# Optimization experiments

Measured on AMD Instinct MI355X. Metric: run time of the kernel, lower is better.

The kernel has to match this reference:

```python
import jax, jax.numpy as jnp
import numpy as np

D_MODEL = 1024
NHEAD = 16
D_K = D_MODEL // NHEAD
CHUNK = 256


def setup_inputs() -> dict:
    key = jax.random.key(0)
    ks = jax.random.split(key, 11)
    S, B = 4096, 4
    inp = {
        "query": jax.random.normal(ks[0], (S, B, D_MODEL), dtype=jnp.float32),
        "key": jax.random.normal(ks[1], (S, B, D_MODEL), dtype=jnp.float32),
        "value": jax.random.normal(ks[2], (S, B, D_MODEL), dtype=jnp.float32),
        # nn.Linear params: y = x @ W.T + b
        "Wq": jax.random.normal(ks[3], (D_MODEL, D_MODEL), dtype=jnp.float32) * 0.02,
        "bq": jnp.zeros((D_MODEL,), dtype=jnp.float32),
        "Wk": jax.random.normal(ks[4], (D_MODEL, D_MODEL), dtype=jnp.float32) * 0.02,
        "bk": jnp.zeros((D_MODEL,), dtype=jnp.float32),
        "Wv": jax.random.normal(ks[5], (D_MODEL, D_MODEL), dtype=jnp.float32) * 0.02,
        "bv": jnp.zeros((D_MODEL,), dtype=jnp.float32),
        "Wo": jax.random.normal(ks[6], (D_MODEL, D_MODEL), dtype=jnp.float32) * 0.02,
        "bo": jnp.zeros((D_MODEL,), dtype=jnp.float32),
    }
    return inp


def _split_heads(x, B):
    # (S, B, D) -> (B, H, S, d_k)
    S = x.shape[0]
    return x.reshape(S, B, NHEAD, D_K).transpose(1, 2, 0, 3)


def reference(query, key, value, Wq, bq, Wk, bk, Wv, bv, Wo, bo):
    S, B, _ = query.shape
    n_chunks = S // CHUNK  # S assumed divisible by CHUNK

    q = _split_heads(query @ Wq.T + bq, B)  # (B,H,S,dk)
    k = _split_heads(key @ Wk.T + bk, B)
    v = _split_heads(value @ Wv.T + bv, B)

    # Block-diagonal attention: softmax is strictly within each chunk.
    qc = q.reshape(B, NHEAD, n_chunks, CHUNK, D_K)
    kc = k.reshape(B, NHEAD, n_chunks, CHUNK, D_K)
    vc = v.reshape(B, NHEAD, n_chunks, CHUNK, D_K)

    scale = 1.0 / np.sqrt(D_K).astype(np.float32)
    scores = jnp.einsum("bhncd,bhnkd->bhnck", qc, kc) * scale  # (B,H,n,C,C)
    probs = jax.nn.softmax(scores, axis=-1)
    out = jnp.einsum("bhnck,bhnkd->bhncd", probs, vc)  # (B,H,n,C,dk)

    # (B,H,S,dk) -> (S,B,H*dk)
    out = out.reshape(B, NHEAD, S, D_K).transpose(2, 0, 1, 3).reshape(S, B, D_MODEL)
    return out @ Wo.T + bo
```

## Files before the change

kernel.cpp:

```cpp
#include <hip/hip_runtime.h>
#include <hip/hip_bf16.h>


namespace {

constexpr int kSeq = 4096, kB = 4, kDm = 1024, kNh = 16, kDk = 64, kChk = 256;
constexpr int kMr = kSeq * kB;
constexpr float kLog2e = 1.44269504088896340736f;

typedef __attribute__((ext_vector_type(8))) short bf16x8;
typedef __attribute__((ext_vector_type(4))) short bf16x4;
typedef __attribute__((ext_vector_type(4))) float f32x4;
typedef __attribute__((ext_vector_type(8))) unsigned short u16x8;
typedef __attribute__((ext_vector_type(4))) unsigned short u16x4;

#define AS1 __attribute__((address_space(1)))
#define AS3 __attribute__((address_space(3)))

__device__ __forceinline__ unsigned short f2bf(float x) {
  union { float f; unsigned u; } v; v.f = x;
  unsigned r = v.u + 0x7fffu + ((v.u >> 16) & 1u);
  return (unsigned short)(r >> 16);
}
__device__ __forceinline__ unsigned cvtpk(float lo, float hi) {
  unsigned r;
  asm("v_cvt_pk_bf16_f32 %0, %1, %2" : "=v"(r) : "v"(lo), "v"(hi));
  return r;
}
__device__ __forceinline__ int swz(int bo) { return bo ^ ((bo >> 3) & 0x70); }

__device__ __forceinline__ f32x4 mfma16x16(bf16x4 a, bf16x4 b, f32x4 c) {
#if __has_builtin(__builtin_amdgcn_mfma_f32_16x16x16bf16_1k)
  return __builtin_amdgcn_mfma_f32_16x16x16bf16_1k(a, b, c, 0, 0, 0);
#else
  asm volatile("v_mfma_f32_16x16x16_bf16 %0, %1, %2, %0\n\ts_nop 4"
               : "+v"(c) : "v"(a), "v"(b));
  return c;
#endif
}

__global__ __launch_bounds__(256) void cvt4(const float* __restrict__ s0,
                                            const float* __restrict__ s1,
                                            const float* __restrict__ s2,
                                            const float* __restrict__ s3,
                                            unsigned short* __restrict__ dst) {
  int i = blockIdx.x * 256 + threadIdx.x;
  int t = i >> 18;
  int j = i & 0x3ffff;
  const float* s = (t == 0) ? s0 : (t == 1) ? s1 : (t == 2) ? s2 : s3;
  f32x4 v = *(const f32x4*)(s + (size_t)j * 4);
  u16x4 o;
  o[0] = f2bf(v[0]); o[1] = f2bf(v[1]); o[2] = f2bf(v[2]); o[3] = f2bf(v[3]);
  *(u16x4*)(dst + (size_t)i * 4) = o;
}

__global__ __launch_bounds__(256) void cvt3(const float* __restrict__ s0,
                                            const float* __restrict__ s1,
                                            const float* __restrict__ s2,
                                            unsigned short* __restrict__ dst) {
  size_t i = (size_t)blockIdx.x * 256 + threadIdx.x;
  int t = (int)(i >> 22);
  size_t j = i & 0x3fffff;
  const float* s = (t == 0) ? s0 : (t == 1) ? s1 : s2;
  f32x4 v = *(const f32x4*)(s + j * 4);
  u16x4 o;
  o[0] = f2bf(v[0]); o[1] = f2bf(v[1]); o[2] = f2bf(v[2]); o[3] = f2bf(v[3]);
  *(u16x4*)(dst + i * 4) = o;
}

__global__ __launch_bounds__(512, 2) void gemm_qkv8(
    const unsigned short* __restrict__ qbf, const unsigned short* __restrict__ kbf,
    const unsigned short* __restrict__ vbf, const unsigned short* __restrict__ Wcat,
    const float* __restrict__ bq, const float* __restrict__ bk,
    const float* __restrict__ bv, unsigned short* __restrict__ dst, float sQ) {
  constexpr int K = kDm, nkt = K / 64;
  __shared__ unsigned short sh[65536];
  const int tid = (int)threadIdx.x;
  const int l = tid & 63;
  const int l15 = l & 15, l4 = l >> 4, l7 = l15 & 7;
  const int wid = tid >> 6, wm = wid >> 2, wn = wid & 3, wn1 = wn & 1;
  const int bid = (int)blockIdx.x;
  const int xcd = bid & 7, idx = bid >> 3;
  const int rbi = xcd * 8 + (idx & 7);
  const int cbi = idx >> 3;
  const int mat = cbi >> 2, ccol = (cbi & 3) * 256;
  const float* bp = (mat == 0) ? bq : (mat == 1) ? bk : bv;
  const float scale = (mat == 0) ? sQ : 1.0f;
  const unsigned short* Ain = (mat == 0) ? qbf : (mat == 1) ? kbf : vbf;
  unsigned short* out = dst + (size_t)mat * kMr * kDm;

  const int srow = tid >> 3;
  const int g16 = (tid & 7) ^ (srow & 7);
  const unsigned short* gA = Ain + (size_t)(rbi * 256 + srow) * K + g16 * 8;
  const unsigned short* gB = Wcat + (size_t)(cbi * 256 + srow) * K + g16 * 8;
  const int ldsbase = (tid & ~63) * 8;

  auto stageA = [&](int T, int h) {
    const unsigned short* s = gA + (size_t)h * (128 * K) + T * 64;
    unsigned short* d = sh + ((T & 1) * 2 + h) * 8192 + ldsbase;
    __builtin_amdgcn_global_load_lds((const AS1 unsigned int*)s, (AS3 unsigned int*)d, 16, 0, 0);
    __builtin_amdgcn_global_load_lds((const AS1 unsigned int*)(s + 64 * K),
                                     (AS3 unsigned int*)(d + 4096), 16, 0, 0);
  };
  auto stageB = [&](int T, int h) {
    const unsigned short* s = gB + (size_t)h * (128 * K) + T * 64;
    unsigned short* d = sh + 32768 + ((T & 1) * 2 + h) * 8192 + ldsbase;
    __builtin_amdgcn_global_load_lds((const AS1 unsigned int*)s, (AS3 unsigned int*)d, 16, 0, 0);
    __builtin_amdgcn_global_load_lds((const AS1 unsigned int*)(s + 64 * K),
                                     (AS3 unsigned int*)(d + 4096), 16, 0, 0);
  };

  f32x4 acc[8][4] = {};
  bf16x8 bfr[4];

  stageB(0, 0); stageB(0, 1);
  stageA(0, 0); stageA(0, 1);
  stageB(1, 0); stageB(1, 1);
  asm volatile("s_waitcnt vmcnt(4)" ::: "memory");
  __builtin_amdgcn_s_barrier();

  for (int it = 0; it < nkt / 2; ++it) {
#pragma unroll
    for (int tt = 0; tt < 2; ++tt) {
      const int T = 2 * it + tt;
      const unsigned short* Asl = sh + ((T & 1) * 2 + wm) * 8192;
      const unsigned short* Bsl = sh + 32768 + ((T & 1) * 2 + (wn >> 1)) * 8192;
#pragma unroll
      for (int p = 0; p < 4; ++p) {
        const int kk = p >> 1, mfh = p & 1;
        bf16x8 af[4];
        const int sc = ((kk * 4 + l4) ^ l7) * 8;
        if (mfh == 0) {
#pragma unroll
          for (int nf = 0; nf < 4; ++nf)
            bfr[nf] = *(const bf16x8*)&Bsl[(wn1 * 64 + nf * 16 + l15) * 64 + sc];
        }
#pragma unroll
        for (int i = 0; i < 4; ++i)
          af[i] = *(const bf16x8*)&Asl[(mfh * 64 + i * 16 + l15) * 64 + sc];
        if (p == 0 && T + 1 < nkt) stageA(T + 1, 0);
        if (p == 1 && T + 1 < nkt) stageA(T + 1, 1);
        if (p == 3 && T + 2 < nkt) { stageB(T + 2, 0); stageB(T + 2, 1); }
        __builtin_amdgcn_s_barrier();
        __builtin_amdgcn_s_setprio(1);
#pragma unroll
        for (int i = 0; i < 4; ++i)
#pragma unroll
          for (int nf = 0; nf < 4; ++nf)
            acc[mfh * 4 + i][nf] =
                __builtin_amdgcn_mfma_f32_16x16x32_bf16(af[i], bfr[nf], acc[mfh * 4 + i][nf], 0, 0, 0);
        __builtin_amdgcn_s_setprio(0);
        if (p == 3 && T + 1 < nkt) {
          if (T + 2 < nkt) asm volatile("s_waitcnt vmcnt(4)" ::: "memory");
          else             asm volatile("s_waitcnt vmcnt(0)" ::: "memory");
        }
        __builtin_amdgcn_s_barrier();
      }
    }
  }

#pragma unroll
  for (int mf = 0; mf < 8; ++mf)
#pragma unroll
    for (int nf = 0; nf < 4; ++nf) {
      int col = wn * 64 + nf * 16 + l15;
      float bvv = bp[ccol + col];
      int grpc = col >> 6;
      int c16 = (col & 63) >> 3, pos = col & 7;
#pragma unroll
      for (int j = 0; j < 4; ++j) {
        int tl = wm * 128 + mf * 16 + l4 * 4 + j;
        int grp = (tl & 3) * 4 + grpc;
        int u = (tl >> 2) * 8 + c16;
        int byte = (grp * 8192 + u * 16 + pos * 2) ^ (((u >> 3) & 7) << 4);
        *(unsigned short*)((char*)sh + byte) = f2bf((acc[mf][nf][j] + bvv) * scale);
      }
    }
  __syncthreads();
  {
    int inner = tid & 31, grp = tid >> 5;
    int b2 = grp >> 2, hl = grp & 3;
    int h = (cbi & 3) * 4 + hl;
    unsigned short* po = out + ((size_t)(b2 * kNh + h) * kSeq + rbi * 64) * kDk;
#pragma unroll
    for (int i = 0; i < 16; ++i) {
      int u = i * 32 + inner;
      int byte = (grp * 8192 + u * 16) ^ (((u >> 3) & 7) << 4);
      u16x8 v = *(const u16x8*)((const char*)sh + byte);
      *(u16x8*)(po + u * 8) = v;
    }
  }
}

__global__ __launch_bounds__(256) void gemm_o(const unsigned short* __restrict__ Aw,
                                              const unsigned short* __restrict__ Bw,
                                              const float* __restrict__ bias,
                                              float* __restrict__ Cp) {
  constexpr int K = kDm, N = kDm;
  __shared__ unsigned short sh[20480];
  const int tid = (int)threadIdx.x;
  const int l = tid & 63;
  const int wbase = tid & ~63;
  const int bid = (int)blockIdx.x;
  const int lin = (bid & 7) * 128 + (bid >> 3);
  const int rb = (lin >> 3) * 128, cb = (lin & 7) * 128;
  const int wr = ((tid >> 7) & 1) * 64;
  const int wc = ((tid >> 6) & 1) * 64;
  const int l15 = l & 15, l4 = l >> 4;

  const int rr0 = tid >> 2;
  const int c4p = (tid & 3) ^ (rr0 & 3);
  const int t0 = rb + rr0, t1 = t0 + 64;
  const unsigned short* gA0 =
      Aw + ((size_t)((t0 & 3) * kNh) * kSeq + (t0 >> 2)) * kDk + c4p * 8;
  const unsigned short* gA1 =
      Aw + ((size_t)((t1 & 3) * kNh) * kSeq + (t1 >> 2)) * kDk + c4p * 8;
  const unsigned short* gB0 = Bw + (size_t)(cb + rr0) * K + c4p * 8;
  const unsigned short* gB1 = gB0 + (size_t)64 * K;
  const int rchk = (l4 ^ (l15 & 3)) * 8;

  f32x4 acc[4][4] = {};

  auto stageA = [&](int slot, int kt) {
    unsigned short* d = sh + slot * 4096;
    size_t ko = (size_t)(kt >> 1) * ((size_t)kSeq * kDk) + (kt & 1) * 32;
    __builtin_amdgcn_global_load_lds((const AS1 unsigned int*)(gA0 + ko),
                                     (AS3 unsigned int*)&d[wbase * 8], 16, 0, 0);
    __builtin_amdgcn_global_load_lds((const AS1 unsigned int*)(gA1 + ko),
                                     (AS3 unsigned int*)&d[(256 + wbase) * 8], 16, 0, 0);
  };
  auto stageB = [&](int slot, int kt) {
    unsigned short* d = sh + 8192 + slot * 4096;
    __builtin_amdgcn_global_load_lds((const AS1 unsigned int*)(gB0 + kt * 32),
                                     (AS3 unsigned int*)&d[wbase * 8], 16, 0, 0);
    __builtin_amdgcn_global_load_lds((const AS1 unsigned int*)(gB1 + kt * 32),
                                     (AS3 unsigned int*)&d[(256 + wbase) * 8], 16, 0, 0);
  };

  constexpr int nkt = K >> 5;
  stageA(0, 0); stageB(0, 0); stageB(1, 1);
  asm volatile("s_waitcnt vmcnt(2)" ::: "memory");
  __builtin_amdgcn_s_barrier();
  __builtin_amdgcn_sched_barrier(0);

  int aR = 0, bR = 0;
  for (int kt = 0; kt < nkt; ++kt) {
    if (kt + 1 < nkt) stageA(aR ^ 1, kt + 1);
    if (kt + 2 < nkt) { int bW = bR + 2; if (bW >= 3) bW -= 3; stageB(bW, kt + 2); }
    const unsigned short* AsC = sh + aR * 4096;
    const unsigned short* BsC = sh + 8192 + bR * 4096;
    bf16x8 af[4], bfr[4];
#pragma unroll
    for (int m = 0; m < 4; ++m)
      af[m] = *(const bf16x8*)&AsC[(wr + m * 16 + l15) * 32 + rchk];
#pragma unroll
    for (int n = 0; n < 4; ++n)
      bfr[n] = *(const bf16x8*)&BsC[(wc + n * 16 + l15) * 32 + rchk];
#pragma unroll
    for (int m = 0; m < 4; ++m)
#pragma unroll
      for (int n = 0; n < 4; ++n)
        acc[m][n] = __builtin_amdgcn_mfma_f32_16x16x32_bf16(af[m], bfr[n], acc[m][n], 0, 0, 0);
    if (kt + 1 < nkt) {
      if (kt + 2 < nkt) asm volatile("s_waitcnt vmcnt(2)" ::: "memory");
      else              asm volatile("s_waitcnt vmcnt(0)" ::: "memory");
      __builtin_amdgcn_s_barrier();
      __builtin_amdgcn_sched_barrier(0);
    }
    aR ^= 1;
    bR = (bR + 1 == 3) ? 0 : bR + 1;
  }

#pragma unroll
  for (int n = 0; n < 4; ++n) {
    int col = cb + wc + n * 16 + l15;
    float bvv = bias[col];
#pragma unroll
    for (int m = 0; m < 4; ++m) {
      int row0 = rb + wr + m * 16 + l4 * 4;
#pragma unroll
      for (int j = 0; j < 4; ++j)
        Cp[(size_t)(row0 + j) * N + col] = acc[m][n][j] + bvv;
    }
  }
}

template <int ALAY, int OHM>
__global__ __launch_bounds__(256) void gemm_bt(const void* __restrict__ Ap,
                                               const unsigned short* __restrict__ Bw,
                                               const float* __restrict__ bias,
                                               void* __restrict__ Cp, float scale) {
  constexpr int K = kDm, N = kDm;
  __shared__ unsigned short As[2][128 * 32];
  __shared__ unsigned short Bs[2][128 * 32];
  const int tid = (int)threadIdx.x;
  const int l = tid & 63;
  const int wbase = tid & ~63;
  const int bid = (int)blockIdx.x;
  const int lin = (bid & 7) * 128 + (bid >> 3);
  const int rb = (lin >> 3) * 128, cb = (lin & 7) * 128;
  const int wr = ((tid >> 7) & 1) * 64;
  const int wc = ((tid >> 6) & 1) * 64;
  const int l15 = l & 15, l4 = l >> 4;

  f32x4 acc[4][4] = {};

  auto stage = [&](int buf, int k0) {
    if constexpr (ALAY == 1) {
      const float* A = (const float*)Ap;
#pragma unroll
      for (int i = 0; i < 4; ++i) {
        int ci = tid + 256 * i;
        int rr = ci >> 3, c4 = ci & 7;
        f32x4 v = *(const f32x4*)(A + (size_t)(rb + rr) * K + (k0 + c4 * 4));
        u16x4 o;
        o[0] = f2bf(v[0]); o[1] = f2bf(v[1]); o[2] = f2bf(v[2]); o[3] = f2bf(v[3]);
        *(u16x4*)&As[buf][rr * 32 + c4 * 4] = o;
      }
    } else {
      const unsigned short* A = (const unsigned short*)Ap;
      int h = k0 >> 6, d0 = k0 & 63;
#pragma unroll
      for (int i = 0; i < 2; ++i) {
        int ch = i * 256 + tid;
        int rr = ch >> 2, cc = ch & 3;
        int t = rb + rr; int s = t >> 2, b2 = t & 3;
        const unsigned short* g =
            A + ((size_t)(b2 * kNh + h) * kSeq + s) * kDk + d0 + cc * 8;
        __builtin_amdgcn_global_load_lds((const AS1 unsigned int*)g,
                                         (AS3 unsigned int*)&As[buf][(i * 256 + wbase) * 8],
                                         16, 0, 0);
      }
    }
#pragma unroll
    for (int i = 0; i < 2; ++i) {
      int ch = i * 256 + tid;
      int rr = ch >> 2, cc = ch & 3;
      const unsigned short* g = Bw + (size_t)(cb + rr) * K + (k0 + cc * 8);
      __builtin_amdgcn_global_load_lds((const AS1 unsigned int*)g,
                                       (AS3 unsigned int*)&Bs[buf][(i * 256 + wbase) * 8],
                                       16, 0, 0);
    }
  };

  stage(0, 0);
  __syncthreads();
  int cur = 0;
  constexpr int nkt = K >> 5;
  for (int kt = 0; kt < nkt; ++kt) {
    if (kt + 1 < nkt) stage(cur ^ 1, (kt + 1) << 5);
    bf16x8 af[4], bfr[4];
#pragma unroll
    for (int m = 0; m < 4; ++m)
      af[m] = *(const bf16x8*)&As[cur][(wr + m * 16 + l15) * 32 + l4 * 8];
#pragma unroll
    for (int n = 0; n < 4; ++n)
      bfr[n] = *(const bf16x8*)&Bs[cur][(wc + n * 16 + l15) * 32 + l4 * 8];
#pragma unroll
    for (int m = 0; m < 4; ++m)
#pragma unroll
      for (int n = 0; n < 4; ++n)
        acc[m][n] = __builtin_amdgcn_mfma_f32_16x16x32_bf16(af[m], bfr[n], acc[m][n], 0, 0, 0);
    __syncthreads();
    cur ^= 1;
  }

#pragma unroll
  for (int n = 0; n < 4; ++n) {
    int col = cb + wc + n * 16 + l15;
    float bvv = bias[col];
    int h = col >> 6, dd = col & 63;
#pragma unroll
    for (int m = 0; m < 4; ++m) {
      int row0 = rb + wr + m * 16 + l4 * 4;
#pragma unroll
      for (int j = 0; j < 4; ++j) {
        float v = acc[m][n][j] + bvv;
        int t = row0 + j;
        if constexpr (OHM) {
          int s = t >> 2, b2 = t & 3;
          ((unsigned short*)Cp)[((size_t)(b2 * kNh + h) * kSeq + s) * kDk + dd] =
              f2bf(v * scale);
        } else {
          ((float*)Cp)[(size_t)t * N + col] = v;
        }
      }
    }
  }
}

__global__ __launch_bounds__(256) void attn_blkdiag(const unsigned short* __restrict__ qw,
                                                    const unsigned short* __restrict__ kw,
                                                    const unsigned short* __restrict__ vw,
                                                    unsigned short* __restrict__ ow) {
  __shared__ unsigned short Kl[64 * 64];
  __shared__ unsigned short Vt[64 * 64];
  const int tid = (int)threadIdx.x;
  const int w = tid >> 6, l = tid & 63;
  const int l15 = l & 15, l4 = l >> 4;
  const int bid0 = (int)blockIdx.x;
  const int bid = (bid0 & 7) * 256 + (bid0 >> 3);
  const int hf = bid & 1, c = (bid >> 1) & 15, bh = bid >> 5;
  const size_t base = ((size_t)bh * kSeq + c * kChk) * kDk;
  const unsigned short* qp = qw + base + (size_t)hf * 128 * kDk;
  const unsigned short* kp = kw + base;
  const unsigned short* vp = vw + base;

  bf16x8 q[2][2];
#pragma unroll
  for (int m = 0; m < 2; ++m)
#pragma unroll
    for (int kk = 0; kk < 2; ++kk)
      q[m][kk] = *(const bf16x8*)(qp + (w * 32 + m * 16 + l15) * 64 + kk * 32 + l4 * 8);

  float mst[2] = {-1e30f, -1e30f}, lst[2] = {0.f, 0.f};
  f32x4 oacc[2][4] = {};

  const int r = tid >> 2, c0 = (tid & 3) * 16;
  u16x8 kr0, kr1, vr0, vr1;
  {
    const unsigned short* kt = kp + tid * 16;
    kr0 = *(const u16x8*)kt; kr1 = *(const u16x8*)(kt + 8);
    const unsigned short* vt = vp + tid * 16;
    vr0 = *(const u16x8*)vt; vr1 = *(const u16x8*)(vt + 8);
  }

  for (int kb = 0; kb < 4; ++kb) {
    __syncthreads();
    {
      int bo = r * 128 + c0 * 2;
      *(u16x8*)((char*)Kl + swz(bo)) = kr0;
      *(u16x8*)((char*)Kl + swz(bo + 16)) = kr1;
#pragma unroll
      for (int j = 0; j < 8; ++j) {
        *(unsigned short*)((char*)Vt + swz((c0 + j) * 128 + r * 2)) = vr0[j];
        *(unsigned short*)((char*)Vt + swz((c0 + 8 + j) * 128 + r * 2)) = vr1[j];
      }
    }
    __syncthreads();
    if (kb < 3) {
      const unsigned short* kt = kp + (kb + 1) * (64 * kDk) + tid * 16;
      kr0 = *(const u16x8*)kt; kr1 = *(const u16x8*)(kt + 8);
      const unsigned short* vt = vp + (kb + 1) * (64 * kDk) + tid * 16;
      vr0 = *(const u16x8*)vt; vr1 = *(const u16x8*)(vt + 8);
    }

    f32x4 sacc[4][2] = {};
    __builtin_amdgcn_s_setprio(1);
#pragma unroll
    for (int kk = 0; kk < 2; ++kk) {
      bf16x8 kf[4];
#pragma unroll
      for (int kn = 0; kn < 4; ++kn) {
        int bo = (kn * 16 + l15) * 128 + (kk * 32 + l4 * 8) * 2;
        kf[kn] = *(const bf16x8*)((const char*)Kl + swz(bo));
      }
#pragma unroll
      for (int kn = 0; kn < 4; ++kn)
#pragma unroll
        for (int m = 0; m < 2; ++m)
          sacc[kn][m] = __builtin_amdgcn_mfma_f32_16x16x32_bf16(kf[kn], q[m][kk], sacc[kn][m], 0, 0, 0);
    }
    __builtin_amdgcn_s_setprio(0);

    unsigned pw[2][4][2];
    float cbq[2][4];
#pragma unroll
    for (int m = 0; m < 2; ++m) {
      float rm = -1e30f;
#pragma unroll
      for (int kn = 0; kn < 4; ++kn)
#pragma unroll
        for (int j = 0; j < 4; ++j) rm = fmaxf(rm, sacc[kn][m][j]);
      rm = fmaxf(rm, __shfl_xor(rm, 16, 64));
      rm = fmaxf(rm, __shfl_xor(rm, 32, 64));
      float mn = fmaxf(mst[m], rm);
      float corr = exp2f(mst[m] - mn);
      mst[m] = mn;
      float rs = 0.f;
#pragma unroll
      for (int kn = 0; kn < 4; ++kn) {
#pragma unroll
        for (int j = 0; j < 4; ++j) {
          float p = exp2f(sacc[kn][m][j] - mn);
          sacc[kn][m][j] = p;
          rs += p;
        }
        pw[m][kn][0] = cvtpk(sacc[kn][m][0], sacc[kn][m][1]);
        pw[m][kn][1] = cvtpk(sacc[kn][m][2], sacc[kn][m][3]);
      }
      rs += __shfl_xor(rs, 16, 64);
      rs += __shfl_xor(rs, 32, 64);
      lst[m] = lst[m] * corr + rs;
#pragma unroll
      for (int j = 0; j < 4; ++j) cbq[m][j] = __shfl(corr, l4 * 4 + j, 64);
#pragma unroll
      for (int n = 0; n < 4; ++n)
#pragma unroll
        for (int j = 0; j < 4; ++j) oacc[m][n][j] *= cbq[m][j];
    }

    __builtin_amdgcn_s_setprio(1);
#pragma unroll
    for (int kn = 0; kn < 4; ++kn) {
      bf16x4 vf[4];
#pragma unroll
      for (int n = 0; n < 4; ++n) {
        int bo = (n * 16 + l15) * 128 + (kn * 16 + l4 * 4) * 2;
        vf[n] = *(const bf16x4*)((const char*)Vt + swz(bo));
      }
#pragma unroll
      for (int m = 0; m < 2; ++m) {
        union { unsigned u[2]; bf16x4 h; } pk;
        pk.u[0] = pw[m][kn][0]; pk.u[1] = pw[m][kn][1];
#pragma unroll
        for (int n = 0; n < 4; ++n)
          oacc[m][n] = mfma16x16(pk.h, vf[n], oacc[m][n]);
      }
    }
    __builtin_amdgcn_s_setprio(0);
  }

  unsigned short* op = ow + base + (size_t)hf * 128 * kDk;
#pragma unroll
  for (int m = 0; m < 2; ++m) {
    float inv = 1.f / lst[m];
#pragma unroll
    for (int j = 0; j < 4; ++j) {
      float ib = __shfl(inv, l4 * 4 + j, 64);
      int srow = w * 32 + m * 16 + l4 * 4 + j;
#pragma unroll
      for (int n = 0; n < 4; ++n)
        op[(size_t)srow * 64 + n * 16 + l15] = f2bf(oacc[m][n][j] * ib);
    }
  }
}

}

extern "C" void kernel_launch(void* const* d_in, const int* in_sizes, int n_in,
                              void* d_out, int out_size, void* d_ws, size_t ws_size,
                              hipStream_t stream) {
  const float* query = (const float*)d_in[0];
  const float* key   = (const float*)d_in[1];
  const float* value = (const float*)d_in[2];
  const float* Wq = (const float*)d_in[3];
  const float* bq = (const float*)d_in[4];
  const float* Wk = (const float*)d_in[5];
  const float* bk = (const float*)d_in[6];
  const float* Wv = (const float*)d_in[7];
  const float* bv = (const float*)d_in[8];
  const float* Wo = (const float*)d_in[9];
  const float* bo = (const float*)d_in[10];

  const float sQ = 0.125f * kLog2e;

  const size_t wsz = (size_t)kDm * kDm;
  const size_t tsz = (size_t)kMr * kDm;
  unsigned short* wsp = (unsigned short*)d_ws;
  unsigned short* wqb = wsp;
  unsigned short* wob = wqb + 3 * wsz;
  unsigned short* qws = wqb + 4 * wsz;
  unsigned short* kws = qws + tsz;
  unsigned short* vws = kws + tsz;
  unsigned short* x0  = vws + tsz;

  const size_t needA = (4 * wsz + 6 * tsz) * 2;
  const size_t needB = (4 * wsz + 4 * tsz) * 2;
  if (ws_size < needB) return;

  cvt4<<<dim3(4096), dim3(256), 0, stream>>>(Wq, Wk, Wv, Wo, wqb);

  if (ws_size >= needA) {
    unsigned short* qbf = x0;
    unsigned short* kbf = qbf + tsz;
    unsigned short* vbf = kbf + tsz;
    unsigned short* aws = qbf;
    cvt3<<<dim3(49152), dim3(256), 0, stream>>>(query, key, value, qbf);
    gemm_qkv8<<<dim3(768), dim3(512), 0, stream>>>(qbf, kbf, vbf, wqb, bq, bk, bv, qws, sQ);
    attn_blkdiag<<<dim3(2048), 256, 0, stream>>>(qws, kws, vws, aws);
    gemm_o<<<dim3(1024), 256, 0, stream>>>(aws, wob, bo, (float*)d_out);
  } else {
    unsigned short* aws = x0;
    gemm_bt<1, 1><<<dim3(1024), 256, 0, stream>>>(query, wqb, bq, qws, sQ);
    gemm_bt<1, 1><<<dim3(1024), 256, 0, stream>>>(key,   wqb + wsz, bk, kws, 1.0f);
    gemm_bt<1, 1><<<dim3(1024), 256, 0, stream>>>(value, wqb + 2 * wsz, bv, vws, 1.0f);
    attn_blkdiag<<<dim3(2048), 256, 0, stream>>>(qws, kws, vws, aws);
    gemm_bt<2, 0><<<dim3(1024), 256, 0, stream>>>(aws, wob, bo, d_out, 1.0f);
  }
}
```

Measured before the change: 271.8 us.

## Rewrite output projection as 256x256-tile 8-wave GEMM and merge conversion kernels

Replaces the 128x128-tile output projection GEMM with a 512-thread kernel computing 256x256 tiles. It uses a 64-wide K step, double-buffered LDS staging via global_load_lds, interleaved prefetch, and setprio around the MFMA blocks, mirroring the QKV GEMM design. This targets better operand reuse and fewer blocks with less per-tile overhead. It also merges the weight and activation fp32-to-bf16 conversions into one launch to drop a kernel launch. The large tile gives only 256 blocks, which may underfill the GPU's compute units.

```diff
diff --git a/kernel.cpp b/kernel.cpp
--- a/kernel.cpp
+++ b/kernel.cpp
@@ -54,18 +54,33 @@
   *(u16x4*)(dst + (size_t)i * 4) = o;
 }
 
-__global__ __launch_bounds__(256) void cvt3(const float* __restrict__ s0,
-                                            const float* __restrict__ s1,
-                                            const float* __restrict__ s2,
-                                            unsigned short* __restrict__ dst) {
+__global__ __launch_bounds__(256) void cvt_all(const float* __restrict__ q,
+                                               const float* __restrict__ k,
+                                               const float* __restrict__ v,
+                                               const float* __restrict__ w0,
+                                               const float* __restrict__ w1,
+                                               const float* __restrict__ w2,
+                                               const float* __restrict__ w3,
+                                               unsigned short* __restrict__ wdst,
+                                               unsigned short* __restrict__ qkvdst) {
   size_t i = (size_t)blockIdx.x * 256 + threadIdx.x;
-  int t = (int)(i >> 22);
-  size_t j = i & 0x3fffff;
-  const float* s = (t == 0) ? s0 : (t == 1) ? s1 : s2;
-  f32x4 v = *(const f32x4*)(s + j * 4);
+  const float* s;
+  unsigned short* d;
+  size_t j;
+  if (i < ((size_t)1 << 20)) {
+    int t = (int)(i >> 18); j = i & 0x3ffff;
+    s = (t == 0) ? w0 : (t == 1) ? w1 : (t == 2) ? w2 : w3;
+    d = wdst + (i << 2);
+  } else {
+    size_t ii = i - ((size_t)1 << 20);
+    int t = (int)(ii >> 22); j = ii & 0x3fffff;
+    s = (t == 0) ? q : (t == 1) ? k : v;
+    d = qkvdst + (ii << 2);
+  }
+  f32x4 vv = *(const f32x4*)(s + j * 4);
   u16x4 o;
-  o[0] = f2bf(v[0]); o[1] = f2bf(v[1]); o[2] = f2bf(v[2]); o[3] = f2bf(v[3]);
-  *(u16x4*)(dst + i * 4) = o;
+  o[0] = f2bf(vv[0]); o[1] = f2bf(vv[1]); o[2] = f2bf(vv[2]); o[3] = f2bf(vv[3]);
+  *(u16x4*)d = o;
 }
 
 __global__ __launch_bounds__(512, 2) void gemm_qkv8(
@@ -192,95 +207,110 @@
   }
 }
 
-__global__ __launch_bounds__(256) void gemm_o(const unsigned short* __restrict__ Aw,
-                                              const unsigned short* __restrict__ Bw,
-                                              const float* __restrict__ bias,
-                                              float* __restrict__ Cp) {
-  constexpr int K = kDm, N = kDm;
-  __shared__ unsigned short sh[20480];
+__global__ __launch_bounds__(512, 2) void gemm_o8(const unsigned short* __restrict__ Aw,
+                                                  const unsigned short* __restrict__ Bw,
+                                                  const float* __restrict__ bias,
+                                                  float* __restrict__ Cp) {
+  constexpr int K = kDm, nkt = K / 64;
+  __shared__ unsigned short sh[65536];
   const int tid = (int)threadIdx.x;
   const int l = tid & 63;
-  const int wbase = tid & ~63;
+  const int l15 = l & 15, l4 = l >> 4, l7 = l15 & 7;
+  const int wid = tid >> 6, wm = wid >> 2, wn = wid & 3, wn1 = wn & 1;
   const int bid = (int)blockIdx.x;
-  const int lin = (bid & 7) * 128 + (bid >> 3);
-  const int rb = (lin >> 3) * 128, cb = (lin & 7) * 128;
-  const int wr = ((tid >> 7) & 1) * 64;
-  const int wc = ((tid >> 6) & 1) * 64;
-  const int l15 = l & 15, l4 = l >> 4;
-
-  const int rr0 = tid >> 2;
-  const int c4p = (tid & 3) ^ (rr0 & 3);
-  const int t0 = rb + rr0, t1 = t0 + 64;
-  const unsigned short* gA0 =
-      Aw + ((size_t)((t0 & 3) * kNh) * kSeq + (t0 >> 2)) * kDk + c4p * 8;
-  const unsigned short* gA1 =
-      Aw + ((size_t)((t1 & 3) * kNh) * kSeq + (t1 >> 2)) * kDk + c4p * 8;
-  const unsigned short* gB0 = Bw + (size_t)(cb + rr0) * K + c4p * 8;
-  const unsigned short* gB1 = gB0 + (size_t)64 * K;
-  const int rchk = (l4 ^ (l15 & 3)) * 8;
-
-  f32x4 acc[4][4] = {};
-
-  auto stageA = [&](int slot, int kt) {
-    unsigned short* d = sh + slot * 4096;
-    size_t ko = (size_t)(kt >> 1) * ((size_t)kSeq * kDk) + (kt & 1) * 32;
-    __builtin_amdgcn_global_load_lds((const AS1 unsigned int*)(gA0 + ko),
-                                     (AS3 unsigned int*)&d[wbase * 8], 16, 0, 0);
-    __builtin_amdgcn_global_load_lds((const AS1 unsigned int*)(gA1 + ko),
-                                     (AS3 unsigned int*)&d[(256 + wbase) * 8], 16, 0, 0);
+  const int xcd = bid & 7, idx = bid >> 3;
+  const int rbi = xcd * 8 + (idx & 7);
+  const int cbi = idx >> 3;
+  const int rb = rbi * 256, cb = cbi * 256;
+
+  const int srow = tid >> 3;
+  const int g16 = (tid & 7) ^ (srow & 7);
+  size_t abase[2][2];
+#pragma unroll
+  for (int h = 0; h < 2; ++h)
+#pragma unroll
+    for (int i = 0; i < 2; ++i) {
+      int t = rb + h * 128 + srow + 64 * i;
+      abase[h][i] = ((size_t)((t & 3) * kNh) * kSeq + (t >> 2)) * kDk + g16 * 8;
+    }
+  const unsigned short* gB = Bw + (size_t)(cb + srow) * K + g16 * 8;
+  const int ldsbase = (tid & ~63) * 8;
+
+  auto stageA = [&](int T, int h) {
+    unsigned short* d = sh + ((T & 1) * 2 + h) * 8192 + ldsbase;
+    size_t ko = (size_t)T * ((size_t)kSeq * kDk);
+    __builtin_amdgcn_global_load_lds((const AS1 unsigned int*)(Aw + abase[h][0] + ko),
+                                     (AS3 unsigned int*)d, 16, 0, 0);
+    __builtin_amdgcn_global_load_lds((const AS1 unsigned int*)(Aw + abase[h][1] + ko),
+                                     (AS3 unsigned int*)(d + 4096), 16, 0, 0);
   };
-  auto stageB = [&](int slot, int kt) {
-    unsigned short* d = sh + 8192 + slot * 4096;
-    __builtin_amdgcn_global_load_lds((const AS1 unsigned int*)(gB0 + kt * 32),
-                                     (AS3 unsigned int*)&d[wbase * 8], 16, 0, 0);
-    __builtin_amdgcn_global_load_lds((const AS1 unsigned int*)(gB1 + kt * 32),
-                                     (AS3 unsigned int*)&d[(256 + wbase) * 8], 16, 0, 0);
+  auto stageB = [&](int T, int h) {
+    const unsigned short* s = gB + (size_t)h * (128 * K) + T * 64;
+    unsigned short* d = sh + 32768 + ((T & 1) * 2 + h) * 8192 + ldsbase;
+    __builtin_amdgcn_global_load_lds((const AS1 unsigned int*)s, (AS3 unsigned int*)d, 16, 0, 0);
+    __builtin_amdgcn_global_load_lds((const AS1 unsigned int*)(s + 64 * K),
+                                     (AS3 unsigned int*)(d + 4096), 16, 0, 0);
   };
 
-  constexpr int nkt = K >> 5;
-  stageA(0, 0); stageB(0, 0); stageB(1, 1);
-  asm volatile("s_waitcnt vmcnt(2)" ::: "memory");
+  f32x4 acc[8][4] = {};
+  bf16x8 bfr[4];
+
+  stageB(0, 0); stageB(0, 1);
+  stageA(0, 0); stageA(0, 1);
+  stageB(1, 0); stageB(1, 1);
+  asm volatile("s_waitcnt vmcnt(4)" ::: "memory");
   __builtin_amdgcn_s_barrier();
-  __builtin_amdgcn_sched_barrier(0);
-
-  int aR = 0, bR = 0;
-  for (int kt = 0; kt < nkt; ++kt) {
-    if (kt + 1 < nkt) stageA(aR ^ 1, kt + 1);
-    if (kt + 2 < nkt) { int bW = bR + 2; if (bW >= 3) bW -= 3; stageB(bW, kt + 2); }
-    const unsigned short* AsC = sh + aR * 4096;
-    const unsigned short* BsC = sh + 8192 + bR * 4096;
-    bf16x8 af[4], bfr[4];
-#pragma unroll
-    for (int m = 0; m < 4; ++m)
-      af[m] = *(const bf16x8*)&AsC[(wr + m * 16 + l15) * 32 + rchk];
-#pragma unroll
-    for (int n = 0; n < 4; ++n)
-      bfr[n] = *(const bf16x8*)&BsC[(wc + n * 16 + l15) * 32 + rchk];
-#pragma unroll
-    for (int m = 0; m < 4; ++m)
-#pragma unroll
-      for (int n = 0; n < 4; ++n)
-        acc[m][n] = __builtin_amdgcn_mfma_f32_16x16x32_bf16(af[m], bfr[n], acc[m][n], 0, 0, 0);
-    if (kt + 1 < nkt) {
-      if (kt + 2 < nkt) asm volatile("s_waitcnt vmcnt(2)" ::: "memory");
-      else              asm volatile("s_waitcnt vmcnt(0)" ::: "memory");
-      __builtin_amdgcn_s_barrier();
-      __builtin_amdgcn_sched_barrier(0);
-    }
-    aR ^= 1;
-    bR = (bR + 1 == 3) ? 0 : bR + 1;
-  }
-
-#pragma unroll
-  for (int n = 0; n < 4; ++n) {
-    int col = cb + wc + n * 16 + l15;
+
+  for (int it = 0; it < nkt / 2; ++it) {
+#pragma unroll
+    for (int tt = 0; tt < 2; ++tt) {
+      const int T = 2 * it + tt;
+      const unsigned short* Asl = sh + ((T & 1) * 2 + wm) * 8192;
+      const unsigned short* Bsl = sh + 32768 + ((T & 1) * 2 + (wn >> 1)) * 8192;
+#pragma unroll
+      for (int p = 0; p < 4; ++p) {
+        const int kk = p >> 1, mfh = p & 1;
+        bf16x8 af[4];
+        const int sc = ((kk * 4 + l4) ^ l7) * 8;
+        if (mfh == 0) {
+#pragma unroll
+          for (int nf = 0; nf < 4; ++nf)
+            bfr[nf] = *(const bf16x8*)&Bsl[(wn1 * 64 + nf * 16 + l15) * 64 + sc];
+        }
+#pragma unroll
+        for (int i = 0; i < 4; ++i)
+          af[i] = *(const bf16x8*)&Asl[(mfh * 64 + i * 16 + l15) * 64 + sc];
+        if (p == 0 && T + 1 < nkt) stageA(T + 1, 0);
+        if (p == 1 && T + 1 < nkt) stageA(T + 1, 1);
+        if (p == 3 && T + 2 < nkt) { stageB(T + 2, 0); stageB(T + 2, 1); }
+        __builtin_amdgcn_s_barrier();
+        __builtin_amdgcn_s_setprio(1);
+#pragma unroll
+        for (int i = 0; i < 4; ++i)
+#pragma unroll
+          for (int nf = 0; nf < 4; ++nf)
+            acc[mfh * 4 + i][nf] =
+                __builtin_amdgcn_mfma_f32_16x16x32_bf16(af[i], bfr[nf], acc[mfh * 4 + i][nf], 0, 0, 0);
+        __builtin_amdgcn_s_setprio(0);
+        if (p == 3 && T + 1 < nkt) {
+          if (T + 2 < nkt) asm volatile("s_waitcnt vmcnt(4)" ::: "memory");
+          else             asm volatile("s_waitcnt vmcnt(0)" ::: "memory");
+        }
+        __builtin_amdgcn_s_barrier();
+      }
+    }
+  }
+
+#pragma unroll
+  for (int nf = 0; nf < 4; ++nf) {
+    int col = cb + wn * 64 + nf * 16 + l15;
     float bvv = bias[col];
 #pragma unroll
-    for (int m = 0; m < 4; ++m) {
-      int row0 = rb + wr + m * 16 + l4 * 4;
+    for (int mf = 0; mf < 8; ++mf) {
+      int row0 = rb + wm * 128 + mf * 16 + l4 * 4;
 #pragma unroll
       for (int j = 0; j < 4; ++j)
-        Cp[(size_t)(row0 + j) * N + col] = acc[m][n][j] + bvv;
+        Cp[(size_t)(row0 + j) * kDm + col] = acc[mf][nf][j] + bvv;
     }
   }
 }
@@ -569,19 +599,19 @@
   const size_t needB = (4 * wsz + 4 * tsz) * 2;
   if (ws_size < needB) return;
 
-  cvt4<<<dim3(4096), dim3(256), 0, stream>>>(Wq, Wk, Wv, Wo, wqb);
-
   if (ws_size >= needA) {
     unsigned short* qbf = x0;
     unsigned short* kbf = qbf + tsz;
     unsigned short* vbf = kbf + tsz;
     unsigned short* aws = qbf;
-    cvt3<<<dim3(49152), dim3(256), 0, stream>>>(query, key, value, qbf);
+    cvt_all<<<dim3(53248), dim3(256), 0, stream>>>(query, key, value, Wq, Wk, Wv, Wo,
+                                                   wqb, qbf);
     gemm_qkv8<<<dim3(768), dim3(512), 0, stream>>>(qbf, kbf, vbf, wqb, bq, bk, bv, qws, sQ);
     attn_blkdiag<<<dim3(2048), 256, 0, stream>>>(qws, kws, vws, aws);
-    gemm_o<<<dim3(1024), 256, 0, stream>>>(aws, wob, bo, (float*)d_out);
+    gemm_o8<<<dim3(256), dim3(512), 0, stream>>>(aws, wob, bo, (float*)d_out);
   } else {
     unsigned short* aws = x0;
+    cvt4<<<dim3(4096), dim3(256), 0, stream>>>(Wq, Wk, Wv, Wo, wqb);
     gemm_bt<1, 1><<<dim3(1024), 256, 0, stream>>>(query, wqb, bq, qws, sQ);
     gemm_bt<1, 1><<<dim3(1024), 256, 0, stream>>>(key,   wqb + wsz, bk, kws, 1.0f);
     gemm_bt<1, 1><<<dim3(1024), 256, 0, stream>>>(value, wqb + 2 * wsz, bv, vws, 1.0f);
```

Measured after the change: 258.8 us. 4.8% less time.
